# Kernel tuning notes

Hardware: AMD Instinct MI355X
Metric: run time of the kernel (lower is better)

Reference implementation:

```python
import jax, jax.numpy as jnp
import numpy as np

EMBED = 256
BATCH = 4096


def setup_inputs() -> dict:
    key = jax.random.key(0)
    ks = jax.random.split(key, 9)
    d = EMBED
    s = 1.0 / np.sqrt(d)
    inp = {
        "x": jax.random.normal(ks[0], (BATCH, d), dtype=jnp.float32),
        "Wq": jax.random.uniform(ks[1], (d, d), jnp.float32, -s, s),
        "bq": jax.random.uniform(ks[2], (d,), jnp.float32, -s, s),
        "Wk": jax.random.uniform(ks[3], (d, d), jnp.float32, -s, s),
        "bk": jax.random.uniform(ks[4], (d,), jnp.float32, -s, s),
        "Wv": jax.random.uniform(ks[5], (d, d), jnp.float32, -s, s),
        "bv": jax.random.uniform(ks[6], (d,), jnp.float32, -s, s),
        "Wo": jax.random.uniform(ks[7], (d, d), jnp.float32, -s, s),
        "bo": jax.random.uniform(ks[8], (d,), jnp.float32, -s, s),
    }
    return inp


def reference(x, Wq, bq, Wk, bk, Wv, bv, Wo, bo):
    # Q,K,V: [B,d]
    Q = x @ Wq.T + bq
    K = x @ Wk.T + bk
    V = x @ Wv.T + bv
    # outer product per sample: [B,d,d]
    energy = Q[:, :, None] * K[:, None, :]
    attention = jax.nn.softmax(energy, axis=-1)          # [B,d,d]
    attention_weights = attention.mean(axis=-1)          # [B,d]
    out = jnp.einsum("bij,bj->bi", attention, V)        # [B,d]
    out = out @ Wo.T + bo                                # [B,d]
    return (attention_weights, out)
```

## Files before the change

### kernel.cpp

```cpp
#include <hip/hip_runtime.h>

#define D     256
#define BATCH 4096
#define NMOM  31

typedef __attribute__((ext_vector_type(8))) short short8;
typedef __attribute__((ext_vector_type(4))) float f32x4;

__constant__ float INVFACT[NMOM] = {
    1.0f, 1.0f, 0.5f,
    1.6666666666666666e-01f, 4.1666666666666664e-02f, 8.3333333333333332e-03f,
    1.3888888888888889e-03f, 1.9841269841269841e-04f, 2.4801587301587302e-05f,
    2.7557319223985893e-06f, 2.7557319223985888e-07f, 2.5052108385441720e-08f,
    2.0876756987868100e-09f, 1.6059043836821613e-10f, 1.1470745597729725e-11f,
    7.6471637318198164e-13f, 4.7794773323873853e-14f, 2.8114572543455206e-15f,
    1.5619206968586225e-16f, 8.2206352466243295e-18f, 4.1103176233121648e-19f,
    1.9572941063391263e-20f, 8.8967913924505741e-22f, 3.8681701706306843e-23f,
    1.6117375710961184e-24f, 6.4469502843844735e-26f, 2.4795962632247972e-27f,
    9.1836898637955460e-29f, 3.2798892370698379e-30f, 1.1309962886447716e-31f,
    3.7699876288159054e-33f };

__device__ __forceinline__ void split8(const float4 f0, const float4 f1,
                                       short8& h, short8& l) {
    float v[8] = {f0.x, f0.y, f0.z, f0.w, f1.x, f1.y, f1.z, f1.w};
#pragma unroll
    for (int i = 0; i < 8; ++i) {
        unsigned int b  = __float_as_uint(v[i]);
        unsigned int hb = b & 0xFFFF0000u;
        h[i] = (short)(b >> 16);
        float lo = v[i] - __uint_as_float(hb);
        l[i] = (short)(__float_as_uint(lo) >> 16);
    }
}

__device__ __forceinline__ void gemm_body(const float* __restrict__ A,
                                          const float* __restrict__ W,
                                          const float* __restrict__ bias,
                                          float* __restrict__ C,
                                          int b0, int n0) {
    __shared__ short Ah[64][40];
    __shared__ short Al[64][40];
    __shared__ short Wh[64][40];
    __shared__ short Wl[64][40];

    const int tid  = threadIdx.x;
    const int lane = tid & 63;
    const int wave = tid >> 6;
    const int wm   = wave >> 1;
    const int wn   = wave & 1;
    const int fr   = lane & 15;
    const int fq   = lane >> 4;

    const int srow = tid >> 2;
    const int sq   = tid & 3;

    f32x4 acc[2][2] = {};

    const float* aBase = A + (size_t)(b0 + srow) * D + sq * 8;
    const float* wBase = W + (size_t)(n0 + srow) * D + sq * 8;

    for (int k0 = 0; k0 < D; k0 += 32) {
        float4 a0 = *(const float4*)(aBase + k0);
        float4 a1 = *(const float4*)(aBase + k0 + 4);
        float4 w0 = *(const float4*)(wBase + k0);
        float4 w1 = *(const float4*)(wBase + k0 + 4);

        __syncthreads();

        short8 h, l;
        split8(a0, a1, h, l);
        *(short8*)&Ah[srow][sq * 8] = h;
        *(short8*)&Al[srow][sq * 8] = l;
        split8(w0, w1, h, l);
        *(short8*)&Wh[srow][sq * 8] = h;
        *(short8*)&Wl[srow][sq * 8] = l;

        __syncthreads();

        short8 arh[2], arl[2], brh[2], brl[2];
#pragma unroll
        for (int mi = 0; mi < 2; ++mi) {
            const int r = wm * 32 + mi * 16 + fr;
            arh[mi] = *(const short8*)&Ah[r][fq * 8];
            arl[mi] = *(const short8*)&Al[r][fq * 8];
        }
#pragma unroll
        for (int ni = 0; ni < 2; ++ni) {
            const int r = wn * 32 + ni * 16 + fr;
            brh[ni] = *(const short8*)&Wh[r][fq * 8];
            brl[ni] = *(const short8*)&Wl[r][fq * 8];
        }
#pragma unroll
        for (int mi = 0; mi < 2; ++mi)
#pragma unroll
            for (int ni = 0; ni < 2; ++ni) {
                acc[mi][ni] = __builtin_amdgcn_mfma_f32_16x16x32_bf16(
                    arh[mi], brl[ni], acc[mi][ni], 0, 0, 0);
                acc[mi][ni] = __builtin_amdgcn_mfma_f32_16x16x32_bf16(
                    arl[mi], brh[ni], acc[mi][ni], 0, 0, 0);
                acc[mi][ni] = __builtin_amdgcn_mfma_f32_16x16x32_bf16(
                    arh[mi], brh[ni], acc[mi][ni], 0, 0, 0);
            }
    }

#pragma unroll
    for (int ni = 0; ni < 2; ++ni) {
        const int col = n0 + wn * 32 + ni * 16 + fr;
        const float bv = bias[col];
#pragma unroll
        for (int mi = 0; mi < 2; ++mi) {
            const int rbase = b0 + wm * 32 + mi * 16 + fq * 4;
#pragma unroll
            for (int r = 0; r < 4; ++r)
                C[(size_t)(rbase + r) * D + col] = acc[mi][ni][r] + bv;
        }
    }
}

__global__ __launch_bounds__(256) void qkv_kernel(
    const float* __restrict__ x,
    const float* __restrict__ Wq, const float* __restrict__ bq,
    const float* __restrict__ Wk, const float* __restrict__ bk,
    const float* __restrict__ Wv, const float* __restrict__ bv,
    float* __restrict__ Qo, float* __restrict__ Ko, float* __restrict__ Vo) {
    const float* W; const float* bias; float* C;
    if (blockIdx.z == 0)      { W = Wq; bias = bq; C = Qo; }
    else if (blockIdx.z == 1) { W = Wk; bias = bk; C = Ko; }
    else                      { W = Wv; bias = bv; C = Vo; }
    gemm_body(x, W, bias, C, blockIdx.x * 64, blockIdx.y * 64);
}

__global__ __launch_bounds__(256) void oproj_kernel(
    const float* __restrict__ A, const float* __restrict__ Wo,
    const float* __restrict__ bo, float* __restrict__ C) {
    gemm_body(A, Wo, bo, C, blockIdx.x * 64, blockIdx.y * 64);
}

__global__ __launch_bounds__(64) void attn_kernel(
    const float* __restrict__ Q, const float* __restrict__ K,
    const float* __restrict__ V, float* __restrict__ out_attn,
    float* __restrict__ attn_w) {
    __shared__ float part[16][65][2];
    __shared__ float coef[NMOM][2];

    const int b = blockIdx.x;
    const int l = threadIdx.x;
    const int c    = l & 31;
    const int half = l >> 5;

    float4 k4 = *(const float4*)&K[(size_t)b * D + 4 * l];
    float4 v4 = *(const float4*)&V[(size_t)b * D + 4 * l];

    float ksum = (k4.x + k4.y) + (k4.z + k4.w);
#pragma unroll
    for (int off = 32; off; off >>= 1) ksum += __shfl_xor(ksum, off);
    const float kbar = ksum * (1.0f / 256.0f);
    float ks[4] = {k4.x - kbar, k4.y - kbar, k4.z - kbar, k4.w - kbar};
    float vs[4] = {v4.x, v4.y, v4.z, v4.w};

    float p[4] = {1.f, 1.f, 1.f, 1.f};

#pragma unroll
    for (int pass = 0; pass < 2; ++pass) {
        const int nlo  = pass ? 16 : 0;
        const int ncnt = pass ? (NMOM - 16) : 16;

        for (int nn = 0; nn < ncnt; ++nn) {
            if (nlo + nn > 0) {
#pragma unroll
                for (int u = 0; u < 4; ++u) p[u] *= ks[u];
            }
            float s = (p[0] + p[1]) + (p[2] + p[3]);
            float m = fmaf(p[0], vs[0],
                      fmaf(p[1], vs[1],
                      fmaf(p[2], vs[2], p[3] * vs[3])));
            part[nn][l][0] = s;
            part[nn][l][1] = m;
        }
        __syncthreads();

        const int nvals = ncnt * 2;
        float acc = 0.f;
        if (c < nvals) {
            const int rn = c >> 1, h = c & 1;
            const float* pp = &part[rn][half * 32][h];
#pragma unroll
            for (int t = 0; t < 32; ++t) acc += pp[2 * t];
        }
        acc += __shfl_xor(acc, 32);
        if (half == 0 && c < nvals) {
            const int n = nlo + (c >> 1);
            coef[n][c & 1] = acc * INVFACT[n];
        }
        __syncthreads();
    }

    float4 q4 = *(const float4*)&Q[(size_t)b * D + 4 * l];
    float qs[4] = {q4.x, q4.y, q4.z, q4.w};
    float de[4], nu[4];
#pragma unroll
    for (int u = 0; u < 4; ++u) {
        de[u] = coef[NMOM - 1][0];
        nu[u] = coef[NMOM - 1][1];
    }
#pragma unroll
    for (int n = NMOM - 2; n >= 0; --n) {
        const float cs = coef[n][0];
        const float cm = coef[n][1];
#pragma unroll
        for (int u = 0; u < 4; ++u) {
            de[u] = fmaf(de[u], qs[u], cs);
            nu[u] = fmaf(nu[u], qs[u], cm);
        }
    }

    float4 o;
    o.x = nu[0] * __builtin_amdgcn_rcpf(de[0]);
    o.y = nu[1] * __builtin_amdgcn_rcpf(de[1]);
    o.z = nu[2] * __builtin_amdgcn_rcpf(de[2]);
    o.w = nu[3] * __builtin_amdgcn_rcpf(de[3]);
    *(float4*)&out_attn[(size_t)b * D + 4 * l] = o;

    float4 w4 = {1.0f/256.0f, 1.0f/256.0f, 1.0f/256.0f, 1.0f/256.0f};
    *(float4*)&attn_w[(size_t)b * D + 4 * l] = w4;
}

extern "C" void kernel_launch(void* const* d_in, const int* in_sizes, int n_in,
                              void* d_out, int out_size, void* d_ws, size_t ws_size,
                              hipStream_t stream) {
    const float* x  = (const float*)d_in[0];
    const float* Wq = (const float*)d_in[1];
    const float* bq = (const float*)d_in[2];
    const float* Wk = (const float*)d_in[3];
    const float* bk = (const float*)d_in[4];
    const float* Wv = (const float*)d_in[5];
    const float* bv = (const float*)d_in[6];
    const float* Wo = (const float*)d_in[7];
    const float* bo = (const float*)d_in[8];

    float* out    = (float*)d_out;
    float* attn_w = out;
    float* out2   = out + (size_t)BATCH * D;

    float* Qb = (float*)d_ws;
    float* Kb = Qb + (size_t)BATCH * D;
    float* Vb = Kb + (size_t)BATCH * D;
    float* Ab = Vb + (size_t)BATCH * D;

    dim3 gqkv(BATCH / 64, D / 64, 3);
    qkv_kernel<<<gqkv, 256, 0, stream>>>(x, Wq, bq, Wk, bk, Wv, bv, Qb, Kb, Vb);

    attn_kernel<<<BATCH, 64, 0, stream>>>(Qb, Kb, Vb, Ab, attn_w);

    dim3 gout(BATCH / 64, D / 64, 1);
    oproj_kernel<<<gout, 256, 0, stream>>>(Ab, Wo, bo, out2);
}
```

Measured before the change: 33.44 us.

## Pre-split inputs and weights into bf16 hi/lo, widen GEMM N tile to 128

```diff
diff --git a/kernel.cpp b/kernel.cpp
--- a/kernel.cpp
+++ b/kernel.cpp
@@ -5,6 +5,7 @@
 #define NMOM  31
 
 typedef __attribute__((ext_vector_type(8))) short short8;
+typedef __attribute__((ext_vector_type(4))) short short4e;
 typedef __attribute__((ext_vector_type(4))) float f32x4;
 
 __constant__ float INVFACT[NMOM] = {
@@ -20,28 +21,53 @@
     9.1836898637955460e-29f, 3.2798892370698379e-30f, 1.1309962886447716e-31f,
     3.7699876288159054e-33f };
 
+__device__ __forceinline__ void split1(float v, short& h, short& l) {
+    unsigned int b = __float_as_uint(v);
+    h = (short)(b >> 16);
+    float lo = v - __uint_as_float(b & 0xFFFF0000u);
+    l = (short)(__float_as_uint(lo) >> 16);
+}
+
 __device__ __forceinline__ void split8(const float4 f0, const float4 f1,
                                        short8& h, short8& l) {
     float v[8] = {f0.x, f0.y, f0.z, f0.w, f1.x, f1.y, f1.z, f1.w};
 #pragma unroll
-    for (int i = 0; i < 8; ++i) {
-        unsigned int b  = __float_as_uint(v[i]);
-        unsigned int hb = b & 0xFFFF0000u;
-        h[i] = (short)(b >> 16);
-        float lo = v[i] - __uint_as_float(hb);
-        l[i] = (short)(__float_as_uint(lo) >> 16);
-    }
-}
-
-__device__ __forceinline__ void gemm_body(const float* __restrict__ A,
-                                          const float* __restrict__ W,
-                                          const float* __restrict__ bias,
-                                          float* __restrict__ C,
-                                          int b0, int n0) {
-    __shared__ short Ah[64][40];
-    __shared__ short Al[64][40];
-    __shared__ short Wh[64][40];
-    __shared__ short Wl[64][40];
+    for (int i = 0; i < 8; ++i) { short hh, ll; split1(v[i], hh, ll); h[i] = hh; l[i] = ll; }
+}
+
+__global__ __launch_bounds__(256) void prep_kernel(
+    const float* __restrict__ x,
+    const float* __restrict__ Wq, const float* __restrict__ Wk,
+    const float* __restrict__ Wv, const float* __restrict__ Wo,
+    short* __restrict__ xh, short* __restrict__ xl,
+    short* __restrict__ wh, short* __restrict__ wl) {
+    const int t  = blockIdx.x * 256 + threadIdx.x;
+    const int NX = BATCH * D / 8;
+    const int NW = D * D / 8;
+    const float* src; short* dh; short* dl; int idx;
+    if (t < NX) { src = x; dh = xh; dl = xl; idx = t; }
+    else {
+        int u = t - NX; int w = u >> 13; idx = u & (NW - 1);
+        if (w == 0)      src = Wq;
+        else if (w == 1) src = Wk;
+        else if (w == 2) src = Wv;
+        else             src = Wo;
+        dh = wh + w * (D * D); dl = wl + w * (D * D);
+    }
+    float4 f0 = ((const float4*)src)[idx * 2];
+    float4 f1 = ((const float4*)src)[idx * 2 + 1];
+    short8 h, l; split8(f0, f1, h, l);
+    ((short8*)dh)[idx] = h;
+    ((short8*)dl)[idx] = l;
+}
+
+__device__ __forceinline__ void gemm_body(
+    const short* __restrict__ AhG, const short* __restrict__ AlG,
+    const short* __restrict__ BhG, const short* __restrict__ BlG,
+    const float* __restrict__ bias, float* __restrict__ C,
+    int b0, int n0) {
+    __shared__ short Ah[64][40], Al[64][40];
+    __shared__ short Bh[128][40], Bl[128][40];
 
     const int tid  = threadIdx.x;
     const int lane = tid & 63;
@@ -51,33 +77,38 @@
     const int fr   = lane & 15;
     const int fq   = lane >> 4;
 
-    const int srow = tid >> 2;
-    const int sq   = tid & 3;
-
-    f32x4 acc[2][2] = {};
-
-    const float* aBase = A + (size_t)(b0 + srow) * D + sq * 8;
-    const float* wBase = W + (size_t)(n0 + srow) * D + sq * 8;
+    const int ar  = tid >> 2;
+    const int as  = (tid & 3) * 8;
+    const int br  = tid >> 1;
+    const int bs  = (tid & 1) * 16;
+
+    f32x4 acc[2][4] = {};
+
+    const short* aH = AhG + (size_t)(b0 + ar) * D + as;
+    const short* aL = AlG + (size_t)(b0 + ar) * D + as;
+    const short* bH = BhG + (size_t)(n0 + br) * D + bs;
+    const short* bL = BlG + (size_t)(n0 + br) * D + bs;
 
     for (int k0 = 0; k0 < D; k0 += 32) {
-        float4 a0 = *(const float4*)(aBase + k0);
-        float4 a1 = *(const float4*)(aBase + k0 + 4);
-        float4 w0 = *(const float4*)(wBase + k0);
-        float4 w1 = *(const float4*)(wBase + k0 + 4);
+        short8 sah = *(const short8*)(aH + k0);
+        short8 sal = *(const short8*)(aL + k0);
+        short8 sbh0 = *(const short8*)(bH + k0);
+        short8 sbh1 = *(const short8*)(bH + k0 + 8);
+        short8 sbl0 = *(const short8*)(bL + k0);
+        short8 sbl1 = *(const short8*)(bL + k0 + 8);
 
         __syncthreads();
 
-        short8 h, l;
-        split8(a0, a1, h, l);
-        *(short8*)&Ah[srow][sq * 8] = h;
-        *(short8*)&Al[srow][sq * 8] = l;
-        split8(w0, w1, h, l);
-        *(short8*)&Wh[srow][sq * 8] = h;
-        *(short8*)&Wl[srow][sq * 8] = l;
+        *(short8*)&Ah[ar][as]      = sah;
+        *(short8*)&Al[ar][as]      = sal;
+        *(short8*)&Bh[br][bs]      = sbh0;
+        *(short8*)&Bh[br][bs + 8]  = sbh1;
+        *(short8*)&Bl[br][bs]      = sbl0;
+        *(short8*)&Bl[br][bs + 8]  = sbl1;
 
         __syncthreads();
 
-        short8 arh[2], arl[2], brh[2], brl[2];
+        short8 arh[2], arl[2], brh[4], brl[4];
 #pragma unroll
         for (int mi = 0; mi < 2; ++mi) {
             const int r = wm * 32 + mi * 16 + fr;
@@ -85,15 +116,15 @@
             arl[mi] = *(const short8*)&Al[r][fq * 8];
         }
 #pragma unroll
-        for (int ni = 0; ni < 2; ++ni) {
-            const int r = wn * 32 + ni * 16 + fr;
-            brh[ni] = *(const short8*)&Wh[r][fq * 8];
-            brl[ni] = *(const short8*)&Wl[r][fq * 8];
+        for (int ni = 0; ni < 4; ++ni) {
+            const int r = wn * 64 + ni * 16 + fr;
+            brh[ni] = *(const short8*)&Bh[r][fq * 8];
+            brl[ni] = *(const short8*)&Bl[r][fq * 8];
         }
 #pragma unroll
         for (int mi = 0; mi < 2; ++mi)
 #pragma unroll
-            for (int ni = 0; ni < 2; ++ni) {
+            for (int ni = 0; ni < 4; ++ni) {
                 acc[mi][ni] = __builtin_amdgcn_mfma_f32_16x16x32_bf16(
                     arh[mi], brl[ni], acc[mi][ni], 0, 0, 0);
                 acc[mi][ni] = __builtin_amdgcn_mfma_f32_16x16x32_bf16(
@@ -104,8 +135,8 @@
     }
 
 #pragma unroll
-    for (int ni = 0; ni < 2; ++ni) {
-        const int col = n0 + wn * 32 + ni * 16 + fr;
+    for (int ni = 0; ni < 4; ++ni) {
+        const int col = n0 + wn * 64 + ni * 16 + fr;
         const float bv = bias[col];
 #pragma unroll
         for (int mi = 0; mi < 2; ++mi) {
@@ -118,27 +149,32 @@
 }
 
 __global__ __launch_bounds__(256) void qkv_kernel(
-    const float* __restrict__ x,
-    const float* __restrict__ Wq, const float* __restrict__ bq,
-    const float* __restrict__ Wk, const float* __restrict__ bk,
-    const float* __restrict__ Wv, const float* __restrict__ bv,
+    const short* __restrict__ xh, const short* __restrict__ xl,
+    const short* __restrict__ wh, const short* __restrict__ wl,
+    const float* __restrict__ bq, const float* __restrict__ bk,
+    const float* __restrict__ bv,
     float* __restrict__ Qo, float* __restrict__ Ko, float* __restrict__ Vo) {
-    const float* W; const float* bias; float* C;
-    if (blockIdx.z == 0)      { W = Wq; bias = bq; C = Qo; }
-    else if (blockIdx.z == 1) { W = Wk; bias = bk; C = Ko; }
-    else                      { W = Wv; bias = bv; C = Vo; }
-    gemm_body(x, W, bias, C, blockIdx.x * 64, blockIdx.y * 64);
+    const float* bias; float* C;
+    const int z = blockIdx.z;
+    if (z == 0)      { bias = bq; C = Qo; }
+    else if (z == 1) { bias = bk; C = Ko; }
+    else             { bias = bv; C = Vo; }
+    gemm_body(xh, xl, wh + z * (D * D), wl + z * (D * D), bias, C,
+              blockIdx.x * 64, blockIdx.y * 128);
 }
 
 __global__ __launch_bounds__(256) void oproj_kernel(
-    const float* __restrict__ A, const float* __restrict__ Wo,
+    const short* __restrict__ Abh, const short* __restrict__ Abl,
+    const short* __restrict__ wh, const short* __restrict__ wl,
     const float* __restrict__ bo, float* __restrict__ C) {
-    gemm_body(A, Wo, bo, C, blockIdx.x * 64, blockIdx.y * 64);
+    gemm_body(Abh, Abl, wh + 3 * (D * D), wl + 3 * (D * D), bo, C,
+              blockIdx.x * 64, blockIdx.y * 128);
 }
 
 __global__ __launch_bounds__(64) void attn_kernel(
     const float* __restrict__ Q, const float* __restrict__ K,
-    const float* __restrict__ V, float* __restrict__ out_attn,
+    const float* __restrict__ V,
+    short* __restrict__ Abh, short* __restrict__ Abl,
     float* __restrict__ attn_w) {
     __shared__ float part[16][65][2];
     __shared__ float coef[NMOM][2];
@@ -214,12 +250,15 @@
         }
     }
 
-    float4 o;
-    o.x = nu[0] * __builtin_amdgcn_rcpf(de[0]);
-    o.y = nu[1] * __builtin_amdgcn_rcpf(de[1]);
-    o.z = nu[2] * __builtin_amdgcn_rcpf(de[2]);
-    o.w = nu[3] * __builtin_amdgcn_rcpf(de[3]);
-    *(float4*)&out_attn[(size_t)b * D + 4 * l] = o;
+    short4e oh, ol;
+#pragma unroll
+    for (int u = 0; u < 4; ++u) {
+        float o = nu[u] * __builtin_amdgcn_rcpf(de[u]);
+        short hh, ll; split1(o, hh, ll);
+        oh[u] = hh; ol[u] = ll;
+    }
+    *(short4e*)&Abh[(size_t)b * D + 4 * l] = oh;
+    *(short4e*)&Abl[(size_t)b * D + 4 * l] = ol;
 
     float4 w4 = {1.0f/256.0f, 1.0f/256.0f, 1.0f/256.0f, 1.0f/256.0f};
     *(float4*)&attn_w[(size_t)b * D + 4 * l] = w4;
@@ -242,16 +281,24 @@
     float* attn_w = out;
     float* out2   = out + (size_t)BATCH * D;
 
-    float* Qb = (float*)d_ws;
-    float* Kb = Qb + (size_t)BATCH * D;
-    float* Vb = Kb + (size_t)BATCH * D;
-    float* Ab = Vb + (size_t)BATCH * D;
-
-    dim3 gqkv(BATCH / 64, D / 64, 3);
-    qkv_kernel<<<gqkv, 256, 0, stream>>>(x, Wq, bq, Wk, bk, Wv, bv, Qb, Kb, Vb);
-
-    attn_kernel<<<BATCH, 64, 0, stream>>>(Qb, Kb, Vb, Ab, attn_w);
-
-    dim3 gout(BATCH / 64, D / 64, 1);
-    oproj_kernel<<<gout, 256, 0, stream>>>(Ab, Wo, bo, out2);
-}
+    char* w = (char*)d_ws;
+    short* xh  = (short*)(w + 0);
+    short* xl  = (short*)(w + (2u << 20));
+    short* wh  = (short*)(w + (4u << 20));
+    short* wl  = (short*)(w + (4u << 20) + (512u << 10));
+    float* Qb  = (float*)(w + (8u << 20));
+    float* Kb  = (float*)(w + (12u << 20));
+    float* Vb  = (float*)(w + (16u << 20));
+    short* Abh = (short*)(w + (20u << 20));
+    short* Abl = (short*)(w + (22u << 20));
+
+    prep_kernel<<<640, 256, 0, stream>>>(x, Wq, Wk, Wv, Wo, xh, xl, wh, wl);
+
+    dim3 gqkv(BATCH / 64, D / 128, 3);
+    qkv_kernel<<<gqkv, 256, 0, stream>>>(xh, xl, wh, wl, bq, bk, bv, Qb, Kb, Vb);
+
+    attn_kernel<<<BATCH, 64, 0, stream>>>(Qb, Kb, Vb, Abh, Abl, attn_w);
+
+    dim3 gout(BATCH / 64, D / 128, 1);
+    oproj_kernel<<<gout, 256, 0, stream>>>(Abh, Abl, wh, wl, bo, out2);
+}
```

After: 41.24 us. 1.23x slower.
